# Kernel tuning notes

Measured on AMD Instinct MI355X. Metric: run time of the kernel, lower is better.

The kernel has to match this reference:

```python
import jax, jax.numpy as jnp
import numpy as np


def setup_inputs() -> dict:
    key = jax.random.key(0)
    k1, k2 = jax.random.split(key)
    inp = jax.random.normal(k1, (16, 64, 64, 64), dtype=jnp.float32)  # (B, D, H, W)
    codebook = jax.random.normal(k2, (1024, 64), dtype=jnp.float32)  # (K, D)
    return {"input": inp, "codebook": codebook}


def reference(input, codebook):
    # input: (B, D, *spatial); codebook: (K, D)
    B, D = input.shape[0], input.shape[1]
    spatial = input.shape[2:]
    # move channel dim last, flatten to tokens: (N, D)
    x = jnp.moveaxis(input, 1, -1).reshape(-1, D)
    # squared L2 distances (cdist^2), computed via expansion to avoid (N,K,D)
    x_sq = jnp.sum(x * x, axis=-1, keepdims=True)            # (N, 1)
    e_sq = jnp.sum(codebook * codebook, axis=-1)             # (K,)
    dist = x_sq - 2.0 * (x @ codebook.T) + e_sq              # (N, K)
    idx = jnp.argmin(dist, axis=-1)                          # (N,)
    quantized = jnp.take(codebook, idx, axis=0)              # (N, D)
    # reshape back to (B, *spatial, D) then move D to axis 1
    out = jnp.moveaxis(quantized.reshape((B,) + spatial + (D,)), -1, 1)
    indices = idx.reshape((B,) + spatial)
    return out, indices
```

## Files before the change

### kernel.cpp

```cpp
#include <hip/hip_runtime.h>


typedef _Float16 v8h  __attribute__((ext_vector_type(8)));
typedef float    v16f __attribute__((ext_vector_type(16)));

constexpr int   D         = 64;
constexpr int   K         = 1024;
constexpr int   HW        = 4096;
constexpr int   DHW       = D * HW;
constexpr int   OUT_ELEMS = 16 * DHW;
constexpr float EPS       = 1e-3f;


__global__ __launch_bounds__(256) void vq_prep(
    const float* __restrict__ cb, _Float16* __restrict__ CH, float* __restrict__ esq)
{
    const int blk = blockIdx.x, tid = threadIdx.x;
    if (blk < 72) {
        const int gid  = blk * 256 + tid;
        const int lane = gid & 63;
        const int fid  = gid >> 6;
        const int t    = fid / 9;
        const int kc   = fid - 9 * t;
        const int l31  = lane & 31;
        const int lh   = lane >> 5;
        const int cw   = t * 32 + l31;
        v8h h;
        if (kc < 8) {
            const int  kk = kc & 3;
            const bool lo = kc >= 4;
            const float* src = cb + cw * D + kk * 16 + lh * 8;
            #pragma unroll
            for (int j = 0; j < 8; ++j) {
                const float v = -2.0f * src[j];
                const _Float16 vh = (_Float16)v;
                h[j] = lo ? (_Float16)(v - (float)vh) : vh;
            }
        } else {
            #pragma unroll
            for (int j = 0; j < 8; ++j) h[j] = (_Float16)0.0f;
            if (lh == 0) {
                const float4* c4 = (const float4*)(cb + cw * D);
                float a0 = 0.f, a1 = 0.f, a2 = 0.f, a3 = 0.f;
                #pragma unroll
                for (int j = 0; j < 16; ++j) {
                    const float4 c = c4[j];
                    a0 = fmaf(c.x, c.x, a0);
                    a1 = fmaf(c.y, c.y, a1);
                    a2 = fmaf(c.z, c.z, a2);
                    a3 = fmaf(c.w, c.w, a3);
                }
                const float e = (a0 + a1) + (a2 + a3);
                const _Float16 ehi = (_Float16)e;
                h[0] = ehi;
                h[1] = (_Float16)(e - (float)ehi);
            }
        }
        *(v8h*)(CH + (size_t)fid * 512 + lane * 8) = h;
    } else {
        const int cw = (blk - 72) * 256 + tid;
        const float4* c4 = (const float4*)(cb + cw * D);
        float a0 = 0.f, a1 = 0.f, a2 = 0.f, a3 = 0.f;
        #pragma unroll
        for (int j = 0; j < 16; ++j) {
            const float4 c = c4[j];
            a0 = fmaf(c.x, c.x, a0);
            a1 = fmaf(c.y, c.y, a1);
            a2 = fmaf(c.z, c.z, a2);
            a3 = fmaf(c.w, c.w, a3);
        }
        esq[cw] = (a0 + a1) + (a2 + a3);
    }
}

__global__ __launch_bounds__(256, 3) void vq_scan(
    const float* __restrict__ input,
    const float* __restrict__ codebook,
    const _Float16* __restrict__ CH,
    const float* __restrict__ esq,
    float* __restrict__ out)
{
    __shared__ _Float16 s_bf[2][2][4][64][8];
    __shared__ float    s_esq[K];
    __shared__ float    s_pv[4][64];
    __shared__ float    s_p2[4][64];
    __shared__ int      s_pk[4][64];
    __shared__ int      s_idx[64];
    __shared__ int      s_list[64];
    __shared__ int      s_cnt;
    __shared__ float    s_xf[64];
    __shared__ float    s_redv[4];
    __shared__ int      s_redk[4];
    __shared__ float    s_q[64][65];

    const int tid  = threadIdx.x;
    const int lane = tid & 63;
    const int q    = __builtin_amdgcn_readfirstlane(tid >> 6);
    const int lh   = lane >> 5;
    const int tok0 = blockIdx.x * 64;
    const int b    = tok0 >> 12;
    const int hwb  = tok0 & 4095;

    if (tid == 0) s_cnt = 0;

    *(float4*)&s_esq[tid * 4] = *(const float4*)&esq[tid * 4];

    {
        const float* xb = input + (size_t)b * DHW + hwb;
        #pragma unroll
        for (int pass = 0; pass < 4; ++pass) {
            const int d   = pass * 16 + (tid >> 4);
            const int hw4 = (tid & 15) * 4;
            const float4 v = *(const float4*)(xb + (size_t)d * HW + hw4);
            const float vv[4] = {v.x, v.y, v.z, v.w};
            #pragma unroll
            for (int u = 0; u < 4; ++u) {
                const int tk = hw4 + u;
                const float f = vv[u];
                const _Float16 fh = (_Float16)f;
                s_bf[0][tk >> 5][d >> 4][((d >> 3) & 1) * 32 + (tk & 31)][d & 7] = fh;
                s_bf[1][tk >> 5][d >> 4][((d >> 3) & 1) * 32 + (tk & 31)][d & 7] =
                    (_Float16)(f - (float)fh);
            }
        }
    }
    __syncthreads();

    v8h bh[2][4], bl[2][4];
    #pragma unroll
    for (int ct = 0; ct < 2; ++ct)
        #pragma unroll
        for (int kc = 0; kc < 4; ++kc) {
            bh[ct][kc] = *(const v8h*)&s_bf[0][ct][kc][lane][0];
            bl[ct][kc] = *(const v8h*)&s_bf[1][ct][kc][lane][0];
        }

    v8h b5;
    #pragma unroll
    for (int j = 0; j < 8; ++j) b5[j] = (_Float16)0.0f;
    if (lh == 0) { b5[0] = (_Float16)1.0f; b5[1] = (_Float16)1.0f; }

    v16f Z = {0,0,0,0,0,0,0,0,0,0,0,0,0,0,0,0};
    const float INF = __builtin_huge_valf();
    float bv0 = INF, b20 = INF, bv1 = INF, b21 = INF;
    int   sl0 = 0, sl1 = 0;

    const v8h* Abase = (const v8h*)CH + lane;

    #pragma unroll 2
    for (int t = 0; t < 8; ++t) {
        const v8h* Ap = Abase + (size_t)((q * 8 + t) * 9) * 64;
        const v8h ah0 = Ap[0],   ah1 = Ap[64],  ah2 = Ap[128], ah3 = Ap[192];
        const v8h al0 = Ap[256], al1 = Ap[320], al2 = Ap[384], al3 = Ap[448];
        const v8h ae  = Ap[512];

        v16f acc0 = __builtin_amdgcn_mfma_f32_32x32x16_f16(ae, b5, Z, 0, 0, 0);
        v16f acc1 = __builtin_amdgcn_mfma_f32_32x32x16_f16(ae, b5, Z, 0, 0, 0);

        acc0 = __builtin_amdgcn_mfma_f32_32x32x16_f16(ah0, bh[0][0], acc0, 0, 0, 0);
        acc1 = __builtin_amdgcn_mfma_f32_32x32x16_f16(ah0, bh[1][0], acc1, 0, 0, 0);
        acc0 = __builtin_amdgcn_mfma_f32_32x32x16_f16(ah1, bh[0][1], acc0, 0, 0, 0);
        acc1 = __builtin_amdgcn_mfma_f32_32x32x16_f16(ah1, bh[1][1], acc1, 0, 0, 0);
        acc0 = __builtin_amdgcn_mfma_f32_32x32x16_f16(ah2, bh[0][2], acc0, 0, 0, 0);
        acc1 = __builtin_amdgcn_mfma_f32_32x32x16_f16(ah2, bh[1][2], acc1, 0, 0, 0);
        acc0 = __builtin_amdgcn_mfma_f32_32x32x16_f16(ah3, bh[0][3], acc0, 0, 0, 0);
        acc1 = __builtin_amdgcn_mfma_f32_32x32x16_f16(ah3, bh[1][3], acc1, 0, 0, 0);

        acc0 = __builtin_amdgcn_mfma_f32_32x32x16_f16(ah0, bl[0][0], acc0, 0, 0, 0);
        acc1 = __builtin_amdgcn_mfma_f32_32x32x16_f16(ah0, bl[1][0], acc1, 0, 0, 0);
        acc0 = __builtin_amdgcn_mfma_f32_32x32x16_f16(ah1, bl[0][1], acc0, 0, 0, 0);
        acc1 = __builtin_amdgcn_mfma_f32_32x32x16_f16(ah1, bl[1][1], acc1, 0, 0, 0);
        acc0 = __builtin_amdgcn_mfma_f32_32x32x16_f16(ah2, bl[0][2], acc0, 0, 0, 0);
        acc1 = __builtin_amdgcn_mfma_f32_32x32x16_f16(ah2, bl[1][2], acc1, 0, 0, 0);
        acc0 = __builtin_amdgcn_mfma_f32_32x32x16_f16(ah3, bl[0][3], acc0, 0, 0, 0);
        acc1 = __builtin_amdgcn_mfma_f32_32x32x16_f16(ah3, bl[1][3], acc1, 0, 0, 0);

        acc0 = __builtin_amdgcn_mfma_f32_32x32x16_f16(al0, bh[0][0], acc0, 0, 0, 0);
        acc1 = __builtin_amdgcn_mfma_f32_32x32x16_f16(al0, bh[1][0], acc1, 0, 0, 0);
        acc0 = __builtin_amdgcn_mfma_f32_32x32x16_f16(al1, bh[0][1], acc0, 0, 0, 0);
        acc1 = __builtin_amdgcn_mfma_f32_32x32x16_f16(al1, bh[1][1], acc1, 0, 0, 0);
        acc0 = __builtin_amdgcn_mfma_f32_32x32x16_f16(al2, bh[0][2], acc0, 0, 0, 0);
        acc1 = __builtin_amdgcn_mfma_f32_32x32x16_f16(al2, bh[1][2], acc1, 0, 0, 0);
        acc0 = __builtin_amdgcn_mfma_f32_32x32x16_f16(al3, bh[0][3], acc0, 0, 0, 0);
        acc1 = __builtin_amdgcn_mfma_f32_32x32x16_f16(al3, bh[1][3], acc1, 0, 0, 0);

        #pragma unroll
        for (int r = 0; r < 16; ++r) {
            const int slot = (t << 4) | r;
            const float s0 = acc0[r];
            b20 = __builtin_amdgcn_fmed3f(s0, bv0, b20);
            if (s0 < bv0) { bv0 = s0; sl0 = slot; }
            const float s1 = acc1[r];
            b21 = __builtin_amdgcn_fmed3f(s1, bv1, b21);
            if (s1 < bv1) { bv1 = s1; sl1 = slot; }
        }
    }

    #pragma unroll
    for (int ct = 0; ct < 2; ++ct) {
        const float bv = ct ? bv1 : bv0;
        const float b2 = ct ? b21 : b20;
        const int   sl = ct ? sl1 : sl0;
        const float obv = __shfl_xor(bv, 32, 64);
        const float ob2 = __shfl_xor(b2, 32, 64);
        const int   osl = __shfl_xor(sl, 32, 64);
        const bool  oth = obv < bv;
        const float B1  = oth ? obv : bv;
        const float B2  = fminf(fmaxf(bv, obv), fminf(b2, ob2));
        const int   wsl = oth ? osl : sl;
        const int   wlh = oth ? (lh ^ 1) : lh;
        const int   r   = wsl & 15;
        const int   tt  = wsl >> 4;
        const int   cw  = (q * 8 + tt) * 32 + (r & 3) + 8 * (r >> 2) + 4 * wlh;
        if (lane < 32) {
            s_pv[q][ct * 32 + lane] = B1;
            s_p2[q][ct * 32 + lane] = B2;
            s_pk[q][ct * 32 + lane] = cw;
        }
    }
    __syncthreads();

    if (tid < 64) {
        float B1 = INF, B2 = INF; int CW = 0;
        #pragma unroll
        for (int qq = 0; qq < 4; ++qq) {
            const float pv = s_pv[qq][tid];
            const float p2 = s_p2[qq][tid];
            const int   pk = s_pk[qq][tid];
            if (pv < B1) { B2 = fminf(B1, p2); B1 = pv; CW = pk; }
            else         { B2 = fminf(B2, pv); }
        }
        s_idx[tid] = CW;
        if (B2 - B1 < EPS) {
            const int p = atomicAdd(&s_cnt, 1);
            s_list[p] = tid;
        }
    }
    __syncthreads();

    {
        const int cnt = s_cnt;
        const int rr  = tid >> 2;
        const int c   = tid & 3;
        for (int ii = 0; ii < cnt; ++ii) {
            const int tl = s_list[ii];
            if (tid < 64) s_xf[tid] = input[(size_t)b * DHW + (size_t)tid * HW + (hwb + tl)];
            __syncthreads();
            const float4* xs4 = (const float4*)&s_xf[c * 16];
            const float4 x0 = xs4[0], x1 = xs4[1], x2 = xs4[2], x3 = xs4[3];
            float bestv = INF; int bestk = K;
            #pragma unroll 4
            for (int i = 0; i < 16; ++i) {
                const int k = i * 64 + rr;
                const float4* c4 = (const float4*)(codebook + (size_t)k * D + c * 16);
                const float4 c0 = c4[0], c1 = c4[1], c2 = c4[2], c3 = c4[3];
                float p0 = 0.f, p1 = 0.f, p2 = 0.f, p3 = 0.f;
                p0 = fmaf(x0.x, c0.x, p0); p0 = fmaf(x0.y, c0.y, p0);
                p0 = fmaf(x0.z, c0.z, p0); p0 = fmaf(x0.w, c0.w, p0);
                p1 = fmaf(x1.x, c1.x, p1); p1 = fmaf(x1.y, c1.y, p1);
                p1 = fmaf(x1.z, c1.z, p1); p1 = fmaf(x1.w, c1.w, p1);
                p2 = fmaf(x2.x, c2.x, p2); p2 = fmaf(x2.y, c2.y, p2);
                p2 = fmaf(x2.z, c2.z, p2); p2 = fmaf(x2.w, c2.w, p2);
                p3 = fmaf(x3.x, c3.x, p3); p3 = fmaf(x3.y, c3.y, p3);
                p3 = fmaf(x3.z, c3.z, p3); p3 = fmaf(x3.w, c3.w, p3);
                float dp = (p0 + p1) + (p2 + p3);
                dp += __shfl_xor(dp, 1, 64);
                dp += __shfl_xor(dp, 2, 64);
                const float s = fmaf(-2.0f, dp, s_esq[k]);
                if (s < bestv) { bestv = s; bestk = k; }
            }
            #pragma unroll
            for (int off = 4; off <= 32; off <<= 1) {
                const float ov = __shfl_xor(bestv, off, 64);
                const int   ok = __shfl_xor(bestk, off, 64);
                if (ov < bestv || (ov == bestv && ok < bestk)) { bestv = ov; bestk = ok; }
            }
            if (lane == 0) { s_redv[q] = bestv; s_redk[q] = bestk; }
            __syncthreads();
            if (tid == 0) {
                float bb = s_redv[0]; int bk = s_redk[0];
                #pragma unroll
                for (int w = 1; w < 4; ++w) {
                    const float v = s_redv[w]; const int kk = s_redk[w];
                    if (v < bb || (v == bb && kk < bk)) { bb = v; bk = kk; }
                }
                s_idx[tl] = bk;
            }
            __syncthreads();
        }
    }

    {
        const int rs  = tid >> 2;
        const int c   = tid & 3;
        const int idx = s_idx[rs];
        const float4* src = (const float4*)(codebook + (size_t)idx * D + c * 16);
        #pragma unroll
        for (int j = 0; j < 4; ++j) {
            const float4 v = src[j];
            float* dst = &s_q[rs][c * 16 + j * 4];
            dst[0] = v.x; dst[1] = v.y; dst[2] = v.z; dst[3] = v.w;
        }
    }
    __syncthreads();
    {
        float* ob = out + (size_t)b * DHW + hwb;
        #pragma unroll
        for (int pass = 0; pass < 4; ++pass) {
            const int d   = pass * 16 + (tid >> 4);
            const int hw4 = (tid & 15) * 4;
            float4 v;
            v.x = s_q[hw4 + 0][d];
            v.y = s_q[hw4 + 1][d];
            v.z = s_q[hw4 + 2][d];
            v.w = s_q[hw4 + 3][d];
            *(float4*)(ob + (size_t)d * HW + hw4) = v;
        }
        if (tid < 64) out[OUT_ELEMS + tok0 + tid] = (float)s_idx[tid];
    }
}

extern "C" void kernel_launch(void* const* d_in, const int* in_sizes, int n_in,
                              void* d_out, int out_size, void* d_ws, size_t ws_size,
                              hipStream_t stream) {
    const float* input    = (const float*)d_in[0];
    const float* codebook = (const float*)d_in[1];
    float* out            = (float*)d_out;

    _Float16* CH  = (_Float16*)d_ws;
    float*    esq = (float*)((char*)d_ws + 294912);

    vq_prep<<<76, 256, 0, stream>>>(codebook, CH, esq);
    vq_scan<<<1024, 256, 0, stream>>>(input, codebook, CH, esq, out);
}
```

Before: 105.9 us.

## Double tokens per block, prefetch codebook tiles, pack slot into distance bits

Each block now handles 128 tokens, with wave pairs splitting the codebook halves. The kernel prefetches the next codebook fragments in registers, rotates the tile start per block to spread L2 traffic, and packs the argmin slot into the low mantissa bits so fminf can replace the compare-and-select. The epilogue writes directly from the codebook without the LDS transpose, and the fixup reads esq from global memory. Packing the slot perturbs the distances, so EPS is widened to send more ambiguous tokens to the exact fp32 fallback. Occupancy drops to 2 blocks per SIMD, and the direct stores are strided per element.

```diff
diff --git a/kernel.cpp b/kernel.cpp
--- a/kernel.cpp
+++ b/kernel.cpp
@@ -9,7 +9,7 @@
 constexpr int   HW        = 4096;
 constexpr int   DHW       = D * HW;
 constexpr int   OUT_ELEMS = 16 * DHW;
-constexpr float EPS       = 1e-3f;
+constexpr float EPS       = 2e-3f;
 
 
 __global__ __launch_bounds__(256) void vq_prep(
@@ -73,53 +73,54 @@
     }
 }
 
-__global__ __launch_bounds__(256, 3) void vq_scan(
+__global__ __launch_bounds__(256, 2) void vq_scan(
     const float* __restrict__ input,
     const float* __restrict__ codebook,
     const _Float16* __restrict__ CH,
     const float* __restrict__ esq,
     float* __restrict__ out)
 {
-    __shared__ _Float16 s_bf[2][2][4][64][8];
-    __shared__ float    s_esq[K];
-    __shared__ float    s_pv[4][64];
-    __shared__ float    s_p2[4][64];
-    __shared__ int      s_pk[4][64];
-    __shared__ int      s_idx[64];
-    __shared__ int      s_list[64];
+    __shared__ _Float16 s_bf[2][2][2][4][64][8];
+    __shared__ float    s_pv[2][2][64];
+    __shared__ float    s_p2[2][2][64];
+    __shared__ int      s_pk[2][2][64];
+    __shared__ int      s_idx[128];
+    __shared__ int      s_list[128];
     __shared__ int      s_cnt;
     __shared__ float    s_xf[64];
     __shared__ float    s_redv[4];
     __shared__ int      s_redk[4];
-    __shared__ float    s_q[64][65];
 
     const int tid  = threadIdx.x;
     const int lane = tid & 63;
     const int q    = __builtin_amdgcn_readfirstlane(tid >> 6);
+    const int g    = q >> 1;
+    const int h    = q & 1;
     const int lh   = lane >> 5;
-    const int tok0 = blockIdx.x * 64;
+    const int tok0 = blockIdx.x * 128;
     const int b    = tok0 >> 12;
     const int hwb  = tok0 & 4095;
+    const int rot  = blockIdx.x & 15;
 
     if (tid == 0) s_cnt = 0;
-
-    *(float4*)&s_esq[tid * 4] = *(const float4*)&esq[tid * 4];
 
     {
         const float* xb = input + (size_t)b * DHW + hwb;
         #pragma unroll
-        for (int pass = 0; pass < 4; ++pass) {
-            const int d   = pass * 16 + (tid >> 4);
-            const int hw4 = (tid & 15) * 4;
+        for (int pass = 0; pass < 8; ++pass) {
+            const int d   = pass * 8 + (tid >> 5);
+            const int hw4 = (tid & 31) * 4;
             const float4 v = *(const float4*)(xb + (size_t)d * HW + hw4);
             const float vv[4] = {v.x, v.y, v.z, v.w};
             #pragma unroll
             for (int u = 0; u < 4; ++u) {
-                const int tk = hw4 + u;
+                const int tk  = hw4 + u;
+                const int gg  = tk >> 6;
+                const int tl6 = tk & 63;
                 const float f = vv[u];
                 const _Float16 fh = (_Float16)f;
-                s_bf[0][tk >> 5][d >> 4][((d >> 3) & 1) * 32 + (tk & 31)][d & 7] = fh;
-                s_bf[1][tk >> 5][d >> 4][((d >> 3) & 1) * 32 + (tk & 31)][d & 7] =
+                s_bf[gg][0][tl6 >> 5][d >> 4][((d >> 3) & 1) * 32 + (tl6 & 31)][d & 7] = fh;
+                s_bf[gg][1][tl6 >> 5][d >> 4][((d >> 3) & 1) * 32 + (tl6 & 31)][d & 7] =
                     (_Float16)(f - (float)fh);
             }
         }
@@ -131,8 +132,8 @@
     for (int ct = 0; ct < 2; ++ct)
         #pragma unroll
         for (int kc = 0; kc < 4; ++kc) {
-            bh[ct][kc] = *(const v8h*)&s_bf[0][ct][kc][lane][0];
-            bl[ct][kc] = *(const v8h*)&s_bf[1][ct][kc][lane][0];
+            bh[ct][kc] = *(const v8h*)&s_bf[g][0][ct][kc][lane][0];
+            bl[ct][kc] = *(const v8h*)&s_bf[g][1][ct][kc][lane][0];
         }
 
     v8h b5;
@@ -143,94 +144,98 @@
     v16f Z = {0,0,0,0,0,0,0,0,0,0,0,0,0,0,0,0};
     const float INF = __builtin_huge_valf();
     float bv0 = INF, b20 = INF, bv1 = INF, b21 = INF;
-    int   sl0 = 0, sl1 = 0;
 
     const v8h* Abase = (const v8h*)CH + lane;
 
-    #pragma unroll 2
-    for (int t = 0; t < 8; ++t) {
-        const v8h* Ap = Abase + (size_t)((q * 8 + t) * 9) * 64;
-        const v8h ah0 = Ap[0],   ah1 = Ap[64],  ah2 = Ap[128], ah3 = Ap[192];
-        const v8h al0 = Ap[256], al1 = Ap[320], al2 = Ap[384], al3 = Ap[448];
-        const v8h ae  = Ap[512];
+    v8h a0, a1, a2, a3, a4, a5, a6, a7, ae;
+    {
+        const int T0 = h * 16 + rot;
+        const v8h* Ap = Abase + (size_t)(T0 * 9) * 64;
+        a0 = Ap[0];   a1 = Ap[64];  a2 = Ap[128]; a3 = Ap[192];
+        a4 = Ap[256]; a5 = Ap[320]; a6 = Ap[384]; a7 = Ap[448];
+        ae = Ap[512];
+    }
+    #pragma unroll 1
+    for (int i = 0; i < 16; ++i) {
+        const int tn = (i < 15) ? ((rot + i + 1) & 15) : rot;
+        const v8h* Apn = Abase + (size_t)((h * 16 + tn) * 9) * 64;
+        v8h n0 = Apn[0],   n1 = Apn[64],  n2 = Apn[128], n3 = Apn[192];
+        v8h n4 = Apn[256], n5 = Apn[320], n6 = Apn[384], n7 = Apn[448];
+        v8h ne = Apn[512];
 
         v16f acc0 = __builtin_amdgcn_mfma_f32_32x32x16_f16(ae, b5, Z, 0, 0, 0);
         v16f acc1 = __builtin_amdgcn_mfma_f32_32x32x16_f16(ae, b5, Z, 0, 0, 0);
 
-        acc0 = __builtin_amdgcn_mfma_f32_32x32x16_f16(ah0, bh[0][0], acc0, 0, 0, 0);
-        acc1 = __builtin_amdgcn_mfma_f32_32x32x16_f16(ah0, bh[1][0], acc1, 0, 0, 0);
-        acc0 = __builtin_amdgcn_mfma_f32_32x32x16_f16(ah1, bh[0][1], acc0, 0, 0, 0);
-        acc1 = __builtin_amdgcn_mfma_f32_32x32x16_f16(ah1, bh[1][1], acc1, 0, 0, 0);
-        acc0 = __builtin_amdgcn_mfma_f32_32x32x16_f16(ah2, bh[0][2], acc0, 0, 0, 0);
-        acc1 = __builtin_amdgcn_mfma_f32_32x32x16_f16(ah2, bh[1][2], acc1, 0, 0, 0);
-        acc0 = __builtin_amdgcn_mfma_f32_32x32x16_f16(ah3, bh[0][3], acc0, 0, 0, 0);
-        acc1 = __builtin_amdgcn_mfma_f32_32x32x16_f16(ah3, bh[1][3], acc1, 0, 0, 0);
-
-        acc0 = __builtin_amdgcn_mfma_f32_32x32x16_f16(ah0, bl[0][0], acc0, 0, 0, 0);
-        acc1 = __builtin_amdgcn_mfma_f32_32x32x16_f16(ah0, bl[1][0], acc1, 0, 0, 0);
-        acc0 = __builtin_amdgcn_mfma_f32_32x32x16_f16(ah1, bl[0][1], acc0, 0, 0, 0);
-        acc1 = __builtin_amdgcn_mfma_f32_32x32x16_f16(ah1, bl[1][1], acc1, 0, 0, 0);
-        acc0 = __builtin_amdgcn_mfma_f32_32x32x16_f16(ah2, bl[0][2], acc0, 0, 0, 0);
-        acc1 = __builtin_amdgcn_mfma_f32_32x32x16_f16(ah2, bl[1][2], acc1, 0, 0, 0);
-        acc0 = __builtin_amdgcn_mfma_f32_32x32x16_f16(ah3, bl[0][3], acc0, 0, 0, 0);
-        acc1 = __builtin_amdgcn_mfma_f32_32x32x16_f16(ah3, bl[1][3], acc1, 0, 0, 0);
-
-        acc0 = __builtin_amdgcn_mfma_f32_32x32x16_f16(al0, bh[0][0], acc0, 0, 0, 0);
-        acc1 = __builtin_amdgcn_mfma_f32_32x32x16_f16(al0, bh[1][0], acc1, 0, 0, 0);
-        acc0 = __builtin_amdgcn_mfma_f32_32x32x16_f16(al1, bh[0][1], acc0, 0, 0, 0);
-        acc1 = __builtin_amdgcn_mfma_f32_32x32x16_f16(al1, bh[1][1], acc1, 0, 0, 0);
-        acc0 = __builtin_amdgcn_mfma_f32_32x32x16_f16(al2, bh[0][2], acc0, 0, 0, 0);
-        acc1 = __builtin_amdgcn_mfma_f32_32x32x16_f16(al2, bh[1][2], acc1, 0, 0, 0);
-        acc0 = __builtin_amdgcn_mfma_f32_32x32x16_f16(al3, bh[0][3], acc0, 0, 0, 0);
-        acc1 = __builtin_amdgcn_mfma_f32_32x32x16_f16(al3, bh[1][3], acc1, 0, 0, 0);
-
+        acc0 = __builtin_amdgcn_mfma_f32_32x32x16_f16(a0, bh[0][0], acc0, 0, 0, 0);
+        acc1 = __builtin_amdgcn_mfma_f32_32x32x16_f16(a0, bh[1][0], acc1, 0, 0, 0);
+        acc0 = __builtin_amdgcn_mfma_f32_32x32x16_f16(a1, bh[0][1], acc0, 0, 0, 0);
+        acc1 = __builtin_amdgcn_mfma_f32_32x32x16_f16(a1, bh[1][1], acc1, 0, 0, 0);
+        acc0 = __builtin_amdgcn_mfma_f32_32x32x16_f16(a2, bh[0][2], acc0, 0, 0, 0);
+        acc1 = __builtin_amdgcn_mfma_f32_32x32x16_f16(a2, bh[1][2], acc1, 0, 0, 0);
+        acc0 = __builtin_amdgcn_mfma_f32_32x32x16_f16(a3, bh[0][3], acc0, 0, 0, 0);
+        acc1 = __builtin_amdgcn_mfma_f32_32x32x16_f16(a3, bh[1][3], acc1, 0, 0, 0);
+
+        acc0 = __builtin_amdgcn_mfma_f32_32x32x16_f16(a0, bl[0][0], acc0, 0, 0, 0);
+        acc1 = __builtin_amdgcn_mfma_f32_32x32x16_f16(a0, bl[1][0], acc1, 0, 0, 0);
+        acc0 = __builtin_amdgcn_mfma_f32_32x32x16_f16(a1, bl[0][1], acc0, 0, 0, 0);
+        acc1 = __builtin_amdgcn_mfma_f32_32x32x16_f16(a1, bl[1][1], acc1, 0, 0, 0);
+        acc0 = __builtin_amdgcn_mfma_f32_32x32x16_f16(a2, bl[0][2], acc0, 0, 0, 0);
+        acc1 = __builtin_amdgcn_mfma_f32_32x32x16_f16(a2, bl[1][2], acc1, 0, 0, 0);
+        acc0 = __builtin_amdgcn_mfma_f32_32x32x16_f16(a3, bl[0][3], acc0, 0, 0, 0);
+        acc1 = __builtin_amdgcn_mfma_f32_32x32x16_f16(a3, bl[1][3], acc1, 0, 0, 0);
+
+        acc0 = __builtin_amdgcn_mfma_f32_32x32x16_f16(a4, bh[0][0], acc0, 0, 0, 0);
+        acc1 = __builtin_amdgcn_mfma_f32_32x32x16_f16(a4, bh[1][0], acc1, 0, 0, 0);
+        acc0 = __builtin_amdgcn_mfma_f32_32x32x16_f16(a5, bh[0][1], acc0, 0, 0, 0);
+        acc1 = __builtin_amdgcn_mfma_f32_32x32x16_f16(a5, bh[1][1], acc1, 0, 0, 0);
+        acc0 = __builtin_amdgcn_mfma_f32_32x32x16_f16(a6, bh[0][2], acc0, 0, 0, 0);
+        acc1 = __builtin_amdgcn_mfma_f32_32x32x16_f16(a6, bh[1][2], acc1, 0, 0, 0);
+        acc0 = __builtin_amdgcn_mfma_f32_32x32x16_f16(a7, bh[0][3], acc0, 0, 0, 0);
+        acc1 = __builtin_amdgcn_mfma_f32_32x32x16_f16(a7, bh[1][3], acc1, 0, 0, 0);
+
+        const int tcur = (rot + i) & 15;
         #pragma unroll
         for (int r = 0; r < 16; ++r) {
-            const int slot = (t << 4) | r;
-            const float s0 = acc0[r];
+            const unsigned slot = (unsigned)((tcur << 4) | r);
+            const float s0 = __uint_as_float((__float_as_uint(acc0[r]) & 0xFFFFFF00u) | slot);
             b20 = __builtin_amdgcn_fmed3f(s0, bv0, b20);
-            if (s0 < bv0) { bv0 = s0; sl0 = slot; }
-            const float s1 = acc1[r];
+            bv0 = fminf(bv0, s0);
+            const float s1 = __uint_as_float((__float_as_uint(acc1[r]) & 0xFFFFFF00u) | slot);
             b21 = __builtin_amdgcn_fmed3f(s1, bv1, b21);
-            if (s1 < bv1) { bv1 = s1; sl1 = slot; }
-        }
+            bv1 = fminf(bv1, s1);
+        }
+        a0 = n0; a1 = n1; a2 = n2; a3 = n3;
+        a4 = n4; a5 = n5; a6 = n6; a7 = n7; ae = ne;
     }
 
     #pragma unroll
     for (int ct = 0; ct < 2; ++ct) {
         const float bv = ct ? bv1 : bv0;
         const float b2 = ct ? b21 : b20;
-        const int   sl = ct ? sl1 : sl0;
         const float obv = __shfl_xor(bv, 32, 64);
         const float ob2 = __shfl_xor(b2, 32, 64);
-        const int   osl = __shfl_xor(sl, 32, 64);
-        const bool  oth = obv < bv;
-        const float B1  = oth ? obv : bv;
-        const float B2  = fminf(fmaxf(bv, obv), fminf(b2, ob2));
-        const int   wsl = oth ? osl : sl;
-        const int   wlh = oth ? (lh ^ 1) : lh;
-        const int   r   = wsl & 15;
-        const int   tt  = wsl >> 4;
-        const int   cw  = (q * 8 + tt) * 32 + (r & 3) + 8 * (r >> 2) + 4 * wlh;
+        const float B1 = fminf(bv, obv);
+        const float B2 = fminf(fmaxf(bv, obv), fminf(b2, ob2));
+        const int   lho = (obv < bv) ? (lh ^ 1) : lh;
+        const unsigned slot = __float_as_uint(B1) & 255u;
+        const int r  = slot & 15;
+        const int tt = slot >> 4;
+        const int cw = (h * 16 + tt) * 32 + (r & 3) + 8 * (r >> 2) + 4 * lho;
         if (lane < 32) {
-            s_pv[q][ct * 32 + lane] = B1;
-            s_p2[q][ct * 32 + lane] = B2;
-            s_pk[q][ct * 32 + lane] = cw;
+            s_pv[h][g][ct * 32 + lane] = B1;
+            s_p2[h][g][ct * 32 + lane] = B2;
+            s_pk[h][g][ct * 32 + lane] = cw;
         }
     }
     __syncthreads();
 
-    if (tid < 64) {
-        float B1 = INF, B2 = INF; int CW = 0;
-        #pragma unroll
-        for (int qq = 0; qq < 4; ++qq) {
-            const float pv = s_pv[qq][tid];
-            const float p2 = s_p2[qq][tid];
-            const int   pk = s_pk[qq][tid];
-            if (pv < B1) { B2 = fminf(B1, p2); B1 = pv; CW = pk; }
-            else         { B2 = fminf(B2, pv); }
-        }
-        s_idx[tid] = CW;
+    if (tid < 128) {
+        const int g2 = tid >> 6, tk = tid & 63;
+        const float v0 = s_pv[0][g2][tk], v1 = s_pv[1][g2][tk];
+        const bool  w1 = v1 < v0;
+        const float B1 = fminf(v0, v1);
+        const float B2 = fminf(fmaxf(v0, v1), fminf(s_p2[0][g2][tk], s_p2[1][g2][tk]));
+        s_idx[tid] = w1 ? s_pk[1][g2][tk] : s_pk[0][g2][tk];
         if (B2 - B1 < EPS) {
             const int p = atomicAdd(&s_cnt, 1);
             s_list[p] = tid;
@@ -244,7 +249,8 @@
         const int c   = tid & 3;
         for (int ii = 0; ii < cnt; ++ii) {
             const int tl = s_list[ii];
-            if (tid < 64) s_xf[tid] = input[(size_t)b * DHW + (size_t)tid * HW + (hwb + tl)];
+            if (tid < 64)
+                s_xf[tid] = input[(size_t)b * DHW + (size_t)tid * HW + (hwb + tl)];
             __syncthreads();
             const float4* xs4 = (const float4*)&s_xf[c * 16];
             const float4 x0 = xs4[0], x1 = xs4[1], x2 = xs4[2], x3 = xs4[3];
@@ -266,7 +272,7 @@
                 float dp = (p0 + p1) + (p2 + p3);
                 dp += __shfl_xor(dp, 1, 64);
                 dp += __shfl_xor(dp, 2, 64);
-                const float s = fmaf(-2.0f, dp, s_esq[k]);
+                const float s = fmaf(-2.0f, dp, esq[k]);
                 if (s < bestv) { bestv = s; bestk = k; }
             }
             #pragma unroll
@@ -291,32 +297,22 @@
     }
 
     {
-        const int rs  = tid >> 2;
-        const int c   = tid & 3;
-        const int idx = s_idx[rs];
-        const float4* src = (const float4*)(codebook + (size_t)idx * D + c * 16);
-        #pragma unroll
-        for (int j = 0; j < 4; ++j) {
-            const float4 v = src[j];
-            float* dst = &s_q[rs][c * 16 + j * 4];
-            dst[0] = v.x; dst[1] = v.y; dst[2] = v.z; dst[3] = v.w;
-        }
-    }
-    __syncthreads();
-    {
-        float* ob = out + (size_t)b * DHW + hwb;
-        #pragma unroll
-        for (int pass = 0; pass < 4; ++pass) {
-            const int d   = pass * 16 + (tid >> 4);
-            const int hw4 = (tid & 15) * 4;
-            float4 v;
-            v.x = s_q[hw4 + 0][d];
-            v.y = s_q[hw4 + 1][d];
-            v.z = s_q[hw4 + 2][d];
-            v.w = s_q[hw4 + 3][d];
-            *(float4*)(ob + (size_t)d * HW + hw4) = v;
-        }
-        if (tid < 64) out[OUT_ELEMS + tok0 + tid] = (float)s_idx[tid];
+        const int token = tid & 127;
+        const int dh    = tid >> 7;
+        const int idx   = s_idx[token];
+        const float4* c4 = (const float4*)(codebook + (size_t)idx * D + dh * 32);
+        float4 cr[8];
+        #pragma unroll
+        for (int j = 0; j < 8; ++j) cr[j] = c4[j];
+        float* ob = out + (size_t)b * DHW + (size_t)dh * 32 * HW + hwb + token;
+        #pragma unroll
+        for (int j = 0; j < 8; ++j) {
+            ob[(size_t)(4 * j + 0) * HW] = cr[j].x;
+            ob[(size_t)(4 * j + 1) * HW] = cr[j].y;
+            ob[(size_t)(4 * j + 2) * HW] = cr[j].z;
+            ob[(size_t)(4 * j + 3) * HW] = cr[j].w;
+        }
+        if (tid < 128) out[OUT_ELEMS + tok0 + tid] = (float)s_idx[tid];
     }
 }
 
@@ -331,5 +327,5 @@
     float*    esq = (float*)((char*)d_ws + 294912);
 
     vq_prep<<<76, 256, 0, stream>>>(codebook, CH, esq);
-    vq_scan<<<1024, 256, 0, stream>>>(input, codebook, CH, esq, out);
+    vq_scan<<<512, 256, 0, stream>>>(input, codebook, CH, esq, out);
 }
```

Result: slower. 112.2 us (+6.0%).

## Shrink shared memory in VQ scan to raise occupancy to four blocks per CU

Applied to the files above, without the earlier changes.

The input tile is now stored raw as float in shared memory, and each lane splits it into fp16 hi/lo pairs when loading MFMA operands. The shared esq copy and the s_q transpose buffer are removed. The fallback exact path reads tokens from the raw tile instead of global memory, and the quantized output is written straight from registers as per-token scalar stores that stay coalesced across lanes. Launch bounds go from 3 to 4 blocks per CU, which gives more latency hiding but leaves fewer registers per thread and risks spills.

```diff
diff --git a/kernel.cpp b/kernel.cpp
--- a/kernel.cpp
+++ b/kernel.cpp
@@ -10,6 +10,7 @@
 constexpr int   DHW       = D * HW;
 constexpr int   OUT_ELEMS = 16 * DHW;
 constexpr float EPS       = 1e-3f;
+constexpr int   RAWS      = 68;
 
 
 __global__ __launch_bounds__(256) void vq_prep(
@@ -73,25 +74,23 @@
     }
 }
 
-__global__ __launch_bounds__(256, 3) void vq_scan(
+__global__ __launch_bounds__(256, 4) void vq_scan(
     const float* __restrict__ input,
     const float* __restrict__ codebook,
     const _Float16* __restrict__ CH,
     const float* __restrict__ esq,
     float* __restrict__ out)
 {
-    __shared__ _Float16 s_bf[2][2][4][64][8];
-    __shared__ float    s_esq[K];
-    __shared__ float    s_pv[4][64];
-    __shared__ float    s_p2[4][64];
-    __shared__ int      s_pk[4][64];
-    __shared__ int      s_idx[64];
-    __shared__ int      s_list[64];
-    __shared__ int      s_cnt;
-    __shared__ float    s_xf[64];
-    __shared__ float    s_redv[4];
-    __shared__ int      s_redk[4];
-    __shared__ float    s_q[64][65];
+    __shared__ float s_raw[64][RAWS];
+    __shared__ float s_pv[4][64];
+    __shared__ float s_p2[4][64];
+    __shared__ int   s_pk[4][64];
+    __shared__ int   s_idx[64];
+    __shared__ int   s_list[64];
+    __shared__ int   s_cnt;
+    __shared__ float s_xf[64];
+    __shared__ float s_redv[4];
+    __shared__ int   s_redk[4];
 
     const int tid  = threadIdx.x;
     const int lane = tid & 63;
@@ -103,41 +102,33 @@
 
     if (tid == 0) s_cnt = 0;
 
-    *(float4*)&s_esq[tid * 4] = *(const float4*)&esq[tid * 4];
-
     {
         const float* xb = input + (size_t)b * DHW + hwb;
         #pragma unroll
         for (int pass = 0; pass < 4; ++pass) {
             const int d   = pass * 16 + (tid >> 4);
             const int hw4 = (tid & 15) * 4;
-            const float4 v = *(const float4*)(xb + (size_t)d * HW + hw4);
-            const float vv[4] = {v.x, v.y, v.z, v.w};
-            #pragma unroll
-            for (int u = 0; u < 4; ++u) {
-                const int tk = hw4 + u;
-                const float f = vv[u];
-                const _Float16 fh = (_Float16)f;
-                s_bf[0][tk >> 5][d >> 4][((d >> 3) & 1) * 32 + (tk & 31)][d & 7] = fh;
-                s_bf[1][tk >> 5][d >> 4][((d >> 3) & 1) * 32 + (tk & 31)][d & 7] =
-                    (_Float16)(f - (float)fh);
-            }
+            *(float4*)&s_raw[d][hw4] = *(const float4*)(xb + (size_t)d * HW + hw4);
         }
     }
     __syncthreads();
 
     v8h bh[2][4], bl[2][4];
     #pragma unroll
-    for (int ct = 0; ct < 2; ++ct)
-        #pragma unroll
-        for (int kc = 0; kc < 4; ++kc) {
-            bh[ct][kc] = *(const v8h*)&s_bf[0][ct][kc][lane][0];
-            bl[ct][kc] = *(const v8h*)&s_bf[1][ct][kc][lane][0];
-        }
-
-    v8h b5;
-    #pragma unroll
-    for (int j = 0; j < 8; ++j) b5[j] = (_Float16)0.0f;
+    for (int ct = 0; ct < 2; ++ct) {
+        const int tok = ct * 32 + (lane & 31);
+        #pragma unroll
+        for (int kc = 0; kc < 4; ++kc)
+            #pragma unroll
+            for (int j = 0; j < 8; ++j) {
+                const float f = s_raw[kc * 16 + lh * 8 + j][tok];
+                const _Float16 fh = (_Float16)f;
+                bh[ct][kc][j] = fh;
+                bl[ct][kc][j] = (_Float16)(f - (float)fh);
+            }
+    }
+
+    v8h b5 = {};
     if (lh == 0) { b5[0] = (_Float16)1.0f; b5[1] = (_Float16)1.0f; }
 
     v16f Z = {0,0,0,0,0,0,0,0,0,0,0,0,0,0,0,0};
@@ -244,7 +235,7 @@
         const int c   = tid & 3;
         for (int ii = 0; ii < cnt; ++ii) {
             const int tl = s_list[ii];
-            if (tid < 64) s_xf[tid] = input[(size_t)b * DHW + (size_t)tid * HW + (hwb + tl)];
+            if (tid < 64) s_xf[tid] = s_raw[tid][tl];
             __syncthreads();
             const float4* xs4 = (const float4*)&s_xf[c * 16];
             const float4 x0 = xs4[0], x1 = xs4[1], x2 = xs4[2], x3 = xs4[3];
@@ -266,7 +257,7 @@
                 float dp = (p0 + p1) + (p2 + p3);
                 dp += __shfl_xor(dp, 1, 64);
                 dp += __shfl_xor(dp, 2, 64);
-                const float s = fmaf(-2.0f, dp, s_esq[k]);
+                const float s = fmaf(-2.0f, dp, esq[k]);
                 if (s < bestv) { bestv = s; bestk = k; }
             }
             #pragma unroll
@@ -291,30 +282,20 @@
     }
 
     {
-        const int rs  = tid >> 2;
-        const int c   = tid & 3;
-        const int idx = s_idx[rs];
-        const float4* src = (const float4*)(codebook + (size_t)idx * D + c * 16);
+        const int token = tid & 63;
+        const int dq    = tid >> 6;
+        const int idx   = s_idx[token];
+        const float4* c4 = (const float4*)(codebook + (size_t)idx * D + dq * 16);
+        float4 cr[4];
+        #pragma unroll
+        for (int j = 0; j < 4; ++j) cr[j] = c4[j];
+        float* ob = out + (size_t)b * DHW + (size_t)dq * 16 * HW + hwb + token;
         #pragma unroll
         for (int j = 0; j < 4; ++j) {
-            const float4 v = src[j];
-            float* dst = &s_q[rs][c * 16 + j * 4];
-            dst[0] = v.x; dst[1] = v.y; dst[2] = v.z; dst[3] = v.w;
-        }
-    }
-    __syncthreads();
-    {
-        float* ob = out + (size_t)b * DHW + hwb;
-        #pragma unroll
-        for (int pass = 0; pass < 4; ++pass) {
-            const int d   = pass * 16 + (tid >> 4);
-            const int hw4 = (tid & 15) * 4;
-            float4 v;
-            v.x = s_q[hw4 + 0][d];
-            v.y = s_q[hw4 + 1][d];
-            v.z = s_q[hw4 + 2][d];
-            v.w = s_q[hw4 + 3][d];
-            *(float4*)(ob + (size_t)d * HW + hw4) = v;
+            ob[(size_t)(4 * j + 0) * HW] = cr[j].x;
+            ob[(size_t)(4 * j + 1) * HW] = cr[j].y;
+            ob[(size_t)(4 * j + 2) * HW] = cr[j].z;
+            ob[(size_t)(4 * j + 3) * HW] = cr[j].w;
         }
         if (tid < 64) out[OUT_ELEMS + tok0 + tid] = (float)s_idx[tid];
     }
```

Result: slower. 137.1 us (+29.4%).
